# Kernel tuning notes

Hardware: AMD Instinct MI355X
Metric: run time of the kernel (lower is better)

Reference implementation:

```python
import jax, jax.numpy as jnp
import numpy as np

IN_FEATURES = 1024
OUT_FEATURES = 1024
B, S = 8, 4096


def setup_inputs() -> dict:
    key = jax.random.key(0)
    kx, kw = jax.random.split(key)
    x = jax.random.normal(kx, (B, S, IN_FEATURES), dtype=jnp.float32)
    # weight initialized as randn * 0.1, shape [out_features, in_features]
    weight = jax.random.normal(kw, (OUT_FEATURES, IN_FEATURES), dtype=jnp.float32) * 0.1
    bias = jnp.zeros((OUT_FEATURES,), dtype=jnp.float32)
    return {"x": x, "weight": weight, "bias": bias}


def reference(x, weight, bias):
    # BitNetLinear eval-mode forward.
    # Weight quantization to ternary {-1, 0, +1} with mean-abs scale.
    w_scale = jnp.mean(jnp.abs(weight))  # scalar
    q_weight = jnp.sign(weight) * (jnp.abs(weight) > 0.5 * w_scale).astype(weight.dtype)
    # Activation quantization to int8 range with global abs-max scale.
    i_scale = jnp.max(jnp.abs(x)) / 127.0  # scalar
    q_input = jnp.clip(jnp.round(x / i_scale), -128.0, 127.0)
    # Float GEMM on quantized values, then dequant with both scales.
    out = jnp.einsum('bsk,ok->bso', q_input, q_weight) * w_scale * i_scale
    out = out + bias  # bias added after dequant, matching the torch code
    return out
```

## Files before the change

kernel.cpp:

```cpp
#include <hip/hip_runtime.h>
#include <stdint.h>


#define MK_M 32768
#define MK_K 1024
#define MK_N 1024

typedef __attribute__((ext_vector_type(4))) int int32x4;

#define WS_MAXP_OFF 64
#define WS_PART_OFF 8448
#define WS_QW_OFF 16384
#define WS_QX_OFF (16384 + (1 << 20))
#define WS_NEEDED (WS_QX_OFF + (size_t)MK_M * MK_K)

__global__ void kprep(const float4* __restrict__ x4, const float4* __restrict__ w4,
                      float* __restrict__ maxp, double* __restrict__ partials, long n4x) {
    const int bid = blockIdx.x;
    if (bid < 2048) {
        float m = 0.f;
        const long stride = 2048L * 256;
        for (long i = (long)bid * 256 + threadIdx.x; i < n4x; i += stride) {
            float4 v = x4[i];
            m = fmaxf(m, fmaxf(fmaxf(fabsf(v.x), fabsf(v.y)), fmaxf(fabsf(v.z), fabsf(v.w))));
        }
        #pragma unroll
        for (int off = 1; off < 64; off <<= 1) m = fmaxf(m, __shfl_xor(m, off));
        __shared__ float sm[4];
        int lane = threadIdx.x & 63, wid = threadIdx.x >> 6;
        if (lane == 0) sm[wid] = m;
        __syncthreads();
        if (threadIdx.x == 0) maxp[bid] = fmaxf(fmaxf(sm[0], sm[1]), fmaxf(sm[2], sm[3]));
    } else {
        double s = 0.0;
        for (int i = (bid - 2048) * 256 + threadIdx.x; i < (1 << 18); i += 64 * 256) {
            float4 v = w4[i];
            s += (double)fabsf(v.x);
            s += (double)fabsf(v.y);
            s += (double)fabsf(v.z);
            s += (double)fabsf(v.w);
        }
        __shared__ double sd[256];
        sd[threadIdx.x] = s;
        __syncthreads();
        for (int h = 128; h > 0; h >>= 1) {
            if ((int)threadIdx.x < h) sd[threadIdx.x] += sd[threadIdx.x + h];
            __syncthreads();
        }
        if (threadIdx.x == 0) partials[bid - 2048] = sd[0];
    }
}

__global__ void kquant_w(const float4* __restrict__ w4, unsigned* __restrict__ qw,
                         const double* __restrict__ partials, float* __restrict__ wscp) {
    __shared__ double sws;
    if (threadIdx.x < 64) {
        double s = partials[threadIdx.x];
        #pragma unroll
        for (int off = 1; off < 64; off <<= 1) s += __shfl_xor(s, off);
        if (threadIdx.x == 0) sws = s;
    }
    __syncthreads();
    float wsc = (float)(sws / 1048576.0);
    if (blockIdx.x == 0 && threadIdx.x == 0) *wscp = wsc;
    float thr = 0.5f * wsc;
    int stride = gridDim.x * blockDim.x;
    for (int i = blockIdx.x * blockDim.x + threadIdx.x; i < (1 << 18); i += stride) {
        float4 v = w4[i];
        int q0 = (fabsf(v.x) > thr) ? (v.x > 0.f ? 1 : -1) : 0;
        int q1 = (fabsf(v.y) > thr) ? (v.y > 0.f ? 1 : -1) : 0;
        int q2 = (fabsf(v.z) > thr) ? (v.z > 0.f ? 1 : -1) : 0;
        int q3 = (fabsf(v.w) > thr) ? (v.w > 0.f ? 1 : -1) : 0;
        qw[i] = (q0 & 0xff) | ((q1 & 0xff) << 8) | ((q2 & 0xff) << 16) | ((q3 & 0xff) << 24);
    }
}

__global__ void kquant_x(const float4* __restrict__ x4, unsigned* __restrict__ qx,
                         const float* __restrict__ maxp, float* __restrict__ iscp, long n4) {
    float m = 0.f;
    #pragma unroll
    for (int j = 0; j < 8; ++j) m = fmaxf(m, maxp[threadIdx.x + 256 * j]);
    #pragma unroll
    for (int off = 1; off < 64; off <<= 1) m = fmaxf(m, __shfl_xor(m, off));
    __shared__ float sm[4];
    int lane = threadIdx.x & 63, wid = threadIdx.x >> 6;
    if (lane == 0) sm[wid] = m;
    __syncthreads();
    float isc = fmaxf(fmaxf(sm[0], sm[1]), fmaxf(sm[2], sm[3])) / 127.0f;
    if (blockIdx.x == 0 && threadIdx.x == 0) *iscp = isc;
    long stride = (long)gridDim.x * blockDim.x;
    for (long i = (long)blockIdx.x * blockDim.x + threadIdx.x; i < n4; i += stride) {
        float4 v = x4[i];
        float q0 = fminf(fmaxf(rintf(v.x / isc), -128.f), 127.f);
        float q1 = fminf(fmaxf(rintf(v.y / isc), -128.f), 127.f);
        float q2 = fminf(fmaxf(rintf(v.z / isc), -128.f), 127.f);
        float q3 = fminf(fmaxf(rintf(v.w / isc), -128.f), 127.f);
        int i0 = (int)q0, i1 = (int)q1, i2 = (int)q2, i3 = (int)q3;
        qx[i] = (i0 & 0xff) | ((i1 & 0xff) << 8) | ((i2 & 0xff) << 16) | ((i3 & 0xff) << 24);
    }
}

__global__ __launch_bounds__(512, 2) void kgemm(
    const char* __restrict__ qx, const char* __restrict__ qw,
    const float* __restrict__ bias, const float* __restrict__ wscp,
    const float* __restrict__ iscp, float* __restrict__ out)
{
    __shared__ __align__(16) char smem[2 * 16384];

    const int t = threadIdx.x;
    const int l = t & 63;
    const int w = t >> 6;
    const int wm = w >> 2;
    const int wn = w & 3;

    const int bid = blockIdx.x;
    const int wg = (bid & 7) * 64 + (bid >> 3);
    const int tm = wg >> 2, tn = wg & 3;
    const long m0 = (long)tm * 256;
    const int n0 = tn * 256;

    const int grow = t >> 2;
    const int gch = (t & 3) ^ ((grow >> 1) & 3);
    const char* gAt = qx + (m0 + grow) * (long)MK_K + gch * 16;

    auto stage = [&](int kt1, int b) {
        char* dst = smem + b * 16384 + t * 16;
        const char* src = gAt + kt1 * 64;
        __builtin_amdgcn_global_load_lds(
            (const __attribute__((address_space(1))) void*)src,
            (__attribute__((address_space(3))) void*)dst, 16, 0, 0);
        __builtin_amdgcn_global_load_lds(
            (const __attribute__((address_space(1))) void*)(src + 128 * (long)MK_K),
            (__attribute__((address_space(3))) void*)(dst + 8192), 16, 0, 0);
    };

    const unsigned vo0 = (unsigned)((n0 + wn * 64 + 0 * 16 + (l & 15)) * MK_K + (l >> 4) * 16);
    const unsigned vo1 = vo0 + 16 * MK_K;
    const unsigned vo2 = vo0 + 32 * MK_K;
    const unsigned vo3 = vo0 + 48 * MK_K;

    int32x4 acc[8][4];
    #pragma unroll
    for (int mi = 0; mi < 8; ++mi)
        #pragma unroll
        for (int ni = 0; ni < 4; ++ni) acc[mi][ni] = (int32x4)0;

    int32x4 bfA[4], bfB[4];

    stage(0, 0);
    {
        const char* sb = qw;
        asm volatile("global_load_dwordx4 %0, %1, %2" : "=v"(bfA[0]) : "v"(vo0), "s"(sb));
        asm volatile("global_load_dwordx4 %0, %1, %2" : "=v"(bfA[1]) : "v"(vo1), "s"(sb));
        asm volatile("global_load_dwordx4 %0, %1, %2" : "=v"(bfA[2]) : "v"(vo2), "s"(sb));
        asm volatile("global_load_dwordx4 %0, %1, %2" : "=v"(bfA[3]) : "v"(vo3), "s"(sb));
    }

    auto body = [&](int kt, int32x4 (&bfc)[4], int32x4 (&bfn)[4]) {
        asm volatile("s_waitcnt vmcnt(4)" ::: "memory");
        __builtin_amdgcn_s_barrier();
        __builtin_amdgcn_sched_barrier(0);

        const char* bufA = smem + (kt & 1) * 16384;
        int32x4 af[8];
        #pragma unroll
        for (int i = 0; i < 8; ++i) {
            int row = wm * 128 + i * 16 + (l & 15);
            int ch = (l >> 4) ^ ((row >> 1) & 3);
            af[i] = *(const int32x4*)(bufA + row * 64 + ch * 16);
        }
        if (kt < 15) {
            stage(kt + 1, (kt + 1) & 1);
            const char* sb = qw + (kt + 1) * 64;
            asm volatile("global_load_dwordx4 %0, %1, %2" : "=v"(bfn[0]) : "v"(vo0), "s"(sb));
            asm volatile("global_load_dwordx4 %0, %1, %2" : "=v"(bfn[1]) : "v"(vo1), "s"(sb));
            asm volatile("global_load_dwordx4 %0, %1, %2" : "=v"(bfn[2]) : "v"(vo2), "s"(sb));
            asm volatile("global_load_dwordx4 %0, %1, %2" : "=v"(bfn[3]) : "v"(vo3), "s"(sb));
            asm volatile("s_waitcnt vmcnt(6) lgkmcnt(0)" ::: "memory");
        } else {
            asm volatile("s_waitcnt vmcnt(0) lgkmcnt(0)" ::: "memory");
        }
        __builtin_amdgcn_sched_barrier(0);
        __builtin_amdgcn_s_setprio(1);
        #pragma unroll
        for (int mi = 0; mi < 8; ++mi)
            #pragma unroll
            for (int ni = 0; ni < 4; ++ni)
                acc[mi][ni] = __builtin_amdgcn_mfma_i32_16x16x64_i8(
                    af[mi], bfc[ni], acc[mi][ni], 0, 0, 0);
        __builtin_amdgcn_s_setprio(0);
    };

    for (int kb = 0; kb < 8; ++kb) {
        body(2 * kb,     bfA, bfB);
        body(2 * kb + 1, bfB, bfA);
    }

    const float wsc = *wscp, isc = *iscp;
    const int crow = (l >> 4) * 4;
    const int ccol = l & 15;
    #pragma unroll
    for (int mi = 0; mi < 8; ++mi) {
        #pragma unroll
        for (int ni = 0; ni < 4; ++ni) {
            long r0 = m0 + wm * 128 + mi * 16 + crow;
            int c = n0 + wn * 64 + ni * 16 + ccol;
            float b = bias[c];
            #pragma unroll
            for (int j = 0; j < 4; ++j) {
                out[(r0 + j) * MK_N + c] = ((float)acc[mi][ni][j] * wsc) * isc + b;
            }
        }
    }
}

extern "C" void kernel_launch(void* const* d_in, const int* in_sizes, int n_in,
                              void* d_out, int out_size, void* d_ws, size_t ws_size,
                              hipStream_t stream) {
    const float* x = (const float*)d_in[0];
    const float* wt = (const float*)d_in[1];
    const float* bias = (const float*)d_in[2];
    float* out = (float*)d_out;

    if (ws_size < WS_NEEDED) return;

    char* ws = (char*)d_ws;
    float* wscp = (float*)(ws + 0);
    float* iscp = (float*)(ws + 4);
    float* maxp = (float*)(ws + WS_MAXP_OFF);
    double* partials = (double*)(ws + WS_PART_OFF);
    char* qw = ws + WS_QW_OFF;
    char* qx = ws + WS_QX_OFF;

    const long n_x = (long)in_sizes[0];
    const long n4_x = n_x >> 2;

    kprep<<<2112, 256, 0, stream>>>((const float4*)x, (const float4*)wt, maxp, partials, n4_x);
    kquant_w<<<256, 256, 0, stream>>>((const float4*)wt, (unsigned*)qw, partials, wscp);
    kquant_x<<<2048, 256, 0, stream>>>((const float4*)x, (unsigned*)qx, maxp, iscp, n4_x);

    const int grid = (MK_M / 256) * (MK_N / 256);
    kgemm<<<grid, 512, 0, stream>>>(qx, qw, bias, wscp, iscp, out);
}
```

Baseline: 120.2 us.

## Shrink GEMM tile to 128x128, stage B through LDS, triple-buffer

The int8 GEMM moves from 256x256 tiles with 512 threads to 128x128 tiles with 256 threads. Both the activation and weight tiles are now staged into LDS with async global-to-LDS loads. Weight fragments are no longer loaded directly into registers from global memory. A three-deep LDS ring prefetches two k-steps ahead, which aims to hide load latency and raise occupancy, but it halves per-block data reuse and adds LDS read traffic for B.

```diff
diff --git a/kernel.cpp b/kernel.cpp
--- a/kernel.cpp
+++ b/kernel.cpp
@@ -100,110 +100,98 @@
     }
 }
 
-__global__ __launch_bounds__(512, 2) void kgemm(
+__global__ __launch_bounds__(256, 3) void kgemm(
     const char* __restrict__ qx, const char* __restrict__ qw,
     const float* __restrict__ bias, const float* __restrict__ wscp,
     const float* __restrict__ iscp, float* __restrict__ out)
 {
-    __shared__ __align__(16) char smem[2 * 16384];
+    __shared__ __align__(16) char smem[3 * 16384];
 
     const int t = threadIdx.x;
     const int l = t & 63;
     const int w = t >> 6;
-    const int wm = w >> 2;
-    const int wn = w & 3;
+    const int wm = w >> 1;
+    const int wn = w & 1;
 
     const int bid = blockIdx.x;
-    const int wg = (bid & 7) * 64 + (bid >> 3);
-    const int tm = wg >> 2, tn = wg & 3;
-    const long m0 = (long)tm * 256;
-    const int n0 = tn * 256;
+    const int wg = (bid & 7) * 256 + (bid >> 3);
+    const int tm = wg >> 3, tn = wg & 7;
+    const long m0 = (long)tm * 128;
+    const int n0 = tn * 128;
 
     const int grow = t >> 2;
-    const int gch = (t & 3) ^ ((grow >> 1) & 3);
+    const int gch = (t & 3) ^ ((t >> 3) & 3);
     const char* gAt = qx + (m0 + grow) * (long)MK_K + gch * 16;
+    const char* gBt = qw + (long)(n0 + grow) * MK_K + gch * 16;
 
     auto stage = [&](int kt1, int b) {
         char* dst = smem + b * 16384 + t * 16;
-        const char* src = gAt + kt1 * 64;
-        __builtin_amdgcn_global_load_lds(
-            (const __attribute__((address_space(1))) void*)src,
+        const char* sa = gAt + kt1 * 64;
+        const char* sb = gBt + kt1 * 64;
+        __builtin_amdgcn_global_load_lds(
+            (const __attribute__((address_space(1))) void*)sa,
             (__attribute__((address_space(3))) void*)dst, 16, 0, 0);
         __builtin_amdgcn_global_load_lds(
-            (const __attribute__((address_space(1))) void*)(src + 128 * (long)MK_K),
+            (const __attribute__((address_space(1))) void*)(sa + 64 * (long)MK_K),
+            (__attribute__((address_space(3))) void*)(dst + 4096), 16, 0, 0);
+        __builtin_amdgcn_global_load_lds(
+            (const __attribute__((address_space(1))) void*)sb,
             (__attribute__((address_space(3))) void*)(dst + 8192), 16, 0, 0);
+        __builtin_amdgcn_global_load_lds(
+            (const __attribute__((address_space(1))) void*)(sb + 64 * (long)MK_K),
+            (__attribute__((address_space(3))) void*)(dst + 12288), 16, 0, 0);
     };
 
-    const unsigned vo0 = (unsigned)((n0 + wn * 64 + 0 * 16 + (l & 15)) * MK_K + (l >> 4) * 16);
-    const unsigned vo1 = vo0 + 16 * MK_K;
-    const unsigned vo2 = vo0 + 32 * MK_K;
-    const unsigned vo3 = vo0 + 48 * MK_K;
-
-    int32x4 acc[8][4];
-    #pragma unroll
-    for (int mi = 0; mi < 8; ++mi)
+    int32x4 acc[4][4];
+    #pragma unroll
+    for (int mi = 0; mi < 4; ++mi)
         #pragma unroll
         for (int ni = 0; ni < 4; ++ni) acc[mi][ni] = (int32x4)0;
 
-    int32x4 bfA[4], bfB[4];
-
     stage(0, 0);
-    {
-        const char* sb = qw;
-        asm volatile("global_load_dwordx4 %0, %1, %2" : "=v"(bfA[0]) : "v"(vo0), "s"(sb));
-        asm volatile("global_load_dwordx4 %0, %1, %2" : "=v"(bfA[1]) : "v"(vo1), "s"(sb));
-        asm volatile("global_load_dwordx4 %0, %1, %2" : "=v"(bfA[2]) : "v"(vo2), "s"(sb));
-        asm volatile("global_load_dwordx4 %0, %1, %2" : "=v"(bfA[3]) : "v"(vo3), "s"(sb));
-    }
-
-    auto body = [&](int kt, int32x4 (&bfc)[4], int32x4 (&bfn)[4]) {
-        asm volatile("s_waitcnt vmcnt(4)" ::: "memory");
+    stage(1, 1);
+
+    #pragma unroll
+    for (int kt = 0; kt < 16; ++kt) {
+        if (kt < 15) asm volatile("s_waitcnt vmcnt(4)" ::: "memory");
+        else         asm volatile("s_waitcnt vmcnt(0)" ::: "memory");
         __builtin_amdgcn_s_barrier();
-        __builtin_amdgcn_sched_barrier(0);
-
-        const char* bufA = smem + (kt & 1) * 16384;
-        int32x4 af[8];
-        #pragma unroll
-        for (int i = 0; i < 8; ++i) {
-            int row = wm * 128 + i * 16 + (l & 15);
+
+        const char* bufA = smem + (kt % 3) * 16384;
+        const char* bufB = bufA + 8192;
+
+        int32x4 af[4], bf[4];
+        #pragma unroll
+        for (int i = 0; i < 4; ++i) {
+            int row = wm * 64 + i * 16 + (l & 15);
             int ch = (l >> 4) ^ ((row >> 1) & 3);
             af[i] = *(const int32x4*)(bufA + row * 64 + ch * 16);
         }
-        if (kt < 15) {
-            stage(kt + 1, (kt + 1) & 1);
-            const char* sb = qw + (kt + 1) * 64;
-            asm volatile("global_load_dwordx4 %0, %1, %2" : "=v"(bfn[0]) : "v"(vo0), "s"(sb));
-            asm volatile("global_load_dwordx4 %0, %1, %2" : "=v"(bfn[1]) : "v"(vo1), "s"(sb));
-            asm volatile("global_load_dwordx4 %0, %1, %2" : "=v"(bfn[2]) : "v"(vo2), "s"(sb));
-            asm volatile("global_load_dwordx4 %0, %1, %2" : "=v"(bfn[3]) : "v"(vo3), "s"(sb));
-            asm volatile("s_waitcnt vmcnt(6) lgkmcnt(0)" ::: "memory");
-        } else {
-            asm volatile("s_waitcnt vmcnt(0) lgkmcnt(0)" ::: "memory");
-        }
-        __builtin_amdgcn_sched_barrier(0);
+        #pragma unroll
+        for (int i = 0; i < 4; ++i) {
+            int row = wn * 64 + i * 16 + (l & 15);
+            int ch = (l >> 4) ^ ((row >> 1) & 3);
+            bf[i] = *(const int32x4*)(bufB + row * 64 + ch * 16);
+        }
+        if (kt < 14) stage(kt + 2, (kt + 2) % 3);
         __builtin_amdgcn_s_setprio(1);
         #pragma unroll
-        for (int mi = 0; mi < 8; ++mi)
+        for (int mi = 0; mi < 4; ++mi)
             #pragma unroll
             for (int ni = 0; ni < 4; ++ni)
                 acc[mi][ni] = __builtin_amdgcn_mfma_i32_16x16x64_i8(
-                    af[mi], bfc[ni], acc[mi][ni], 0, 0, 0);
+                    af[mi], bf[ni], acc[mi][ni], 0, 0, 0);
         __builtin_amdgcn_s_setprio(0);
-    };
-
-    for (int kb = 0; kb < 8; ++kb) {
-        body(2 * kb,     bfA, bfB);
-        body(2 * kb + 1, bfB, bfA);
     }
 
     const float wsc = *wscp, isc = *iscp;
     const int crow = (l >> 4) * 4;
     const int ccol = l & 15;
     #pragma unroll
-    for (int mi = 0; mi < 8; ++mi) {
+    for (int mi = 0; mi < 4; ++mi) {
         #pragma unroll
         for (int ni = 0; ni < 4; ++ni) {
-            long r0 = m0 + wm * 128 + mi * 16 + crow;
+            long r0 = m0 + wm * 64 + mi * 16 + crow;
             int c = n0 + wn * 64 + ni * 16 + ccol;
             float b = bias[c];
             #pragma unroll
@@ -239,6 +227,6 @@
     kquant_w<<<256, 256, 0, stream>>>((const float4*)wt, (unsigned*)qw, partials, wscp);
     kquant_x<<<2048, 256, 0, stream>>>((const float4*)x, (unsigned*)qx, maxp, iscp, n4_x);
 
-    const int grid = (MK_M / 256) * (MK_N / 256);
-    kgemm<<<grid, 512, 0, stream>>>(qx, qw, bias, wscp, iscp, out);
-}
+    const int grid = (MK_M / 128) * (MK_N / 128);
+    kgemm<<<grid, 256, 0, stream>>>(qx, qw, bias, wscp, iscp, out);
+}
```

After: 110.6 us. -8.0%, faster.
